# Performance work log

Measured on AMD Instinct MI355X. Metric: run time of the kernel, lower is better.

## Reference

```python
import jax, jax.numpy as jnp
import numpy as np

B, IN_CH, D, H, W = 2, 4, 8, 224, 224
DS = 4
DIM, HEADS, HEAD_DIM, LAYERS = 256, 8, 32, 4
INNER = HEADS * HEAD_DIM
MLP = 4 * DIM
WS = (4, 8, 8)
SHIFT = (2, 4, 4)
WVOL = WS[0] * WS[1] * WS[2]
Hp, Wp = H // DS, W // DS
NW = (D // WS[0]) * (Hp // WS[1]) * (Wp // WS[2])
NBIAS = (2 * WS[0] - 1) * (2 * WS[1] - 1) * (2 * WS[2] - 1)


def _rel_index():
    c = np.stack(np.meshgrid(np.arange(WS[0]), np.arange(WS[1]), np.arange(WS[2]), indexing='ij')).reshape(3, -1)
    r = (c[:, :, None] - c[:, None, :]).transpose(1, 2, 0)
    r[..., 0] += WS[0] - 1
    r[..., 1] += WS[1] - 1
    r[..., 2] += WS[2] - 1
    return r[..., 0] * (2 * WS[1] - 1) * (2 * WS[2] - 1) + r[..., 1] * (2 * WS[2] - 1) + r[..., 2]

REL_IDX = jnp.asarray(_rel_index())  # (WVOL, WVOL)


def _shift_mask():
    # standard Swin shifted-window attention mask on the post-merge grid
    img = np.zeros((D, Hp, Wp), np.int32)
    cnt = 0
    sl = lambda w, s: (slice(0, -w), slice(-w, -s), slice(-s, None))
    for sd in sl(WS[0], SHIFT[0]):
        for sh in sl(WS[1], SHIFT[1]):
            for sw in sl(WS[2], SHIFT[2]):
                img[sd, sh, sw] = cnt
                cnt += 1
    m = img.reshape(D // WS[0], WS[0], Hp // WS[1], WS[1], Wp // WS[2], WS[2])
    m = m.transpose(0, 2, 4, 1, 3, 5).reshape(NW, WVOL)
    return jnp.asarray(np.where(m[:, None, :] != m[:, :, None], -1e9, 0.0).astype(np.float32))

ATTN_MASK = _shift_mask()  # (NW, WVOL, WVOL)


def layer_norm(x, s, b):
    mu = x.mean(-1, keepdims=True)
    var = x.var(-1, keepdims=True)
    return (x - mu) / jnp.sqrt(var + 1e-5) * s + b


def window_attention(x, qkv_w, out_w, out_b, bias_tab, shifted):
    # x: (B, D, Hp, Wp, C) channel-last
    if shifted:
        x = jnp.roll(x, (-SHIFT[0], -SHIFT[1], -SHIFT[2]), axis=(1, 2, 3))
    xw = x.reshape(B, D // WS[0], WS[0], Hp // WS[1], WS[1], Wp // WS[2], WS[2], DIM)
    xw = xw.transpose(0, 1, 3, 5, 2, 4, 6, 7).reshape(B, NW, WVOL, DIM)
    qkv = xw @ qkv_w  # (B, NW, WVOL, 3*INNER)
    q, k, v = jnp.split(qkv, 3, axis=-1)
    split = lambda t: t.reshape(B, NW, WVOL, HEADS, HEAD_DIM).transpose(0, 1, 3, 2, 4)
    q = split(q) * (HEAD_DIM ** -0.5)
    k, v = split(k), split(v)
    attn = jnp.einsum('bwhid,bwhjd->bwhij', q, k)  # (B, NW, H, WVOL, WVOL)
    bias = bias_tab[REL_IDX].transpose(2, 0, 1)  # (H, WVOL, WVOL)
    attn = attn + bias
    if shifted:
        attn = attn + ATTN_MASK[None, :, None]
    attn = jax.nn.softmax(attn, axis=-1)
    o = jnp.einsum('bwhij,bwhjd->bwhid', attn, v)
    o = o.transpose(0, 1, 3, 2, 4).reshape(B, NW, WVOL, INNER)
    o = o @ out_w + out_b
    o = o.reshape(B, D // WS[0], Hp // WS[1], Wp // WS[2], WS[0], WS[1], WS[2], DIM)
    o = o.transpose(0, 1, 4, 2, 5, 3, 6, 7).reshape(B, D, Hp, Wp, DIM)
    if shifted:
        o = jnp.roll(o, SHIFT, axis=(1, 2, 3))
    return o


def setup_inputs() -> dict:
    key = jax.random.key(0)
    ks = jax.random.split(key, 12)
    s = 0.02
    return {
        'x': jax.random.normal(ks[0], (B, IN_CH, D, H, W), jnp.float32),
        'conv_w': jax.random.normal(ks[1], (DIM, IN_CH, 1, DS, DS), jnp.float32) * s,
        'conv_b': jnp.zeros((DIM,), jnp.float32),
        'ln1_s': jnp.ones((LAYERS, DIM), jnp.float32),
        'ln1_b': jnp.zeros((LAYERS, DIM), jnp.float32),
        'qkv_w': jax.random.normal(ks[2], (LAYERS, DIM, 3 * INNER), jnp.float32) * s,
        'out_w': jax.random.normal(ks[3], (LAYERS, INNER, DIM), jnp.float32) * s,
        'out_b': jnp.zeros((LAYERS, DIM), jnp.float32),
        'bias_tab': jax.random.normal(ks[4], (LAYERS, NBIAS, HEADS), jnp.float32) * s,
        'ln2_s': jnp.ones((LAYERS, DIM), jnp.float32),
        'ln2_b': jnp.zeros((LAYERS, DIM), jnp.float32),
        'fc1_w': jax.random.normal(ks[5], (LAYERS, DIM, MLP), jnp.float32) * s,
        'fc1_b': jnp.zeros((LAYERS, MLP), jnp.float32),
        'fc2_w': jax.random.normal(ks[6], (LAYERS, MLP, DIM), jnp.float32) * s,
        'fc2_b': jnp.zeros((LAYERS, DIM), jnp.float32),
    }


def reference(x, conv_w, conv_b, ln1_s, ln1_b, qkv_w, out_w, out_b, bias_tab, ln2_s, ln2_b, fc1_w, fc1_b, fc2_w, fc2_b):
    # patch merge: Conv3d kernel (1, DS, DS) stride (1, DS, DS)
    y = jax.lax.conv_general_dilated(
        x, conv_w, window_strides=(1, DS, DS), padding='VALID',
        dimension_numbers=('NCDHW', 'OIDHW', 'NCDHW'))
    y = y + conv_b[None, :, None, None, None]
    y = y.transpose(0, 2, 3, 4, 1)  # (B, D, Hp, Wp, DIM) channel-last
    for i in range(LAYERS):
        shifted = (i % 2 == 1)
        y = y + window_attention(layer_norm(y, ln1_s[i], ln1_b[i]),
                                 qkv_w[i], out_w[i], out_b[i], bias_tab[i], shifted)
        h = layer_norm(y, ln2_s[i], ln2_b[i])
        h = jax.nn.gelu(h @ fc1_w[i] + fc1_b[i]) @ fc2_w[i] + fc2_b[i]
        y = y + h
    return y.transpose(0, 4, 1, 2, 3)  # (B, DIM, D, Hp, Wp)
```

## Files before the change

kernel.cpp:

```cpp
#include <hip/hip_runtime.h>

typedef unsigned short ushort_t;
typedef unsigned int   uint_t;

#define NTOK 50176
#define NWIN 98
#define NBIAS 1575

typedef __attribute__((ext_vector_type(8))) short bf16x8;
typedef __attribute__((ext_vector_type(4))) float floatx4;

static __device__ __forceinline__ float b2f(ushort_t u) {
    return __uint_as_float(((uint_t)u) << 16);
}
static __device__ __forceinline__ ushort_t f2b(float f) {
    union { float f; uint_t u; } v; v.f = f;
    uint_t u = v.u + 0x7fffu + ((v.u >> 16) & 1u);
    return (ushort_t)(u >> 16);
}

static __device__ __forceinline__ int wtok2tok(int wt, int sh) {
    int b = wt / 25088, rem = wt - b * 25088;
    int win = rem >> 8, pos = rem & 255;
    int wd = win / 49, r1 = win - wd * 49;
    int wh = r1 / 7, ww = r1 - wh * 7;
    int d = wd * 4 + (pos >> 6), h = wh * 8 + ((pos >> 3) & 7), w = ww * 8 + (pos & 7);
    if (sh) { d = (d + 2) & 7; h += 4; if (h >= 56) h -= 56; w += 4; if (w >= 56) w -= 56; }
    return (b * 8 + d) * 3136 + h * 56 + w;
}

__global__ void transpose_w(const float* __restrict__ src, ushort_t* __restrict__ dst,
                            int K, int N) {
    long base = (long)blockIdx.y * K * N;
    int idx = blockIdx.x * 256 + threadIdx.x;
    if (idx < K * N) {
        int k = idx / N, n = idx - k * N;
        dst[base + (long)n * K + k] = f2b(src[base + idx]);
    }
}

__global__ void cast_bf16(const float* __restrict__ src, ushort_t* __restrict__ dst, int n) {
    int i = blockIdx.x * 256 + threadIdx.x;
    if (i < n) dst[i] = f2b(src[i]);
}

__global__ void expand_bias(const float* __restrict__ bias_tab, ushort_t* __restrict__ Bx) {
    int j = blockIdx.x, hd = blockIdx.y, l = blockIdx.z;
    int i = threadIdx.x;
    int rd = (i >> 6) - (j >> 6) + 3;
    int rh = ((i >> 3) & 7) - ((j >> 3) & 7) + 7;
    int rw = (i & 7) - (j & 7) + 7;
    int idx = rd * 225 + rh * 15 + rw;
    Bx[((((size_t)l * 8 + hd) << 8) + j) * 256 + i] =
        f2b(bias_tab[((size_t)l * NBIAS + idx) * 8 + hd]);
}

__global__ void im2row(const float* __restrict__ X, ushort_t* __restrict__ A) {
    int idx = blockIdx.x * 256 + threadIdx.x;
    int t = idx >> 4;
    int k = idx & 15;
    int ic = k >> 2, kh = k & 3;
    int w = t % 56, h = (t / 56) % 56, d = (t / 3136) % 8, b = t / 25088;
    long xi = (((long)(b * 4 + ic) * 8 + d) * 224 + (h * 4 + kh)) * 224 + w * 4;
    float4 u = *(const float4*)(X + xi);
    ushort_t* ap = A + (long)t * 64 + ic * 16 + kh * 4;
    ap[0] = f2b(u.x); ap[1] = f2b(u.y); ap[2] = f2b(u.z); ap[3] = f2b(u.w);
}

__global__ void ln_kernel(const float* __restrict__ Y, ushort_t* __restrict__ Xn,
                          const float* __restrict__ S, const float* __restrict__ Bb) {
    int wv = threadIdx.x >> 6, lane = threadIdx.x & 63;
    long t = (long)blockIdx.x * 4 + wv;
    const float* y = Y + t * 256;
    float v[4], s = 0.f, s2 = 0.f;
#pragma unroll
    for (int r = 0; r < 4; ++r) { v[r] = y[lane + 64 * r]; s += v[r]; s2 += v[r] * v[r]; }
#pragma unroll
    for (int off = 32; off; off >>= 1) { s += __shfl_xor(s, off, 64); s2 += __shfl_xor(s2, off, 64); }
    float mu = s * (1.f / 256.f);
    float var = s2 * (1.f / 256.f) - mu * mu;
    float rstd = rsqrtf(var + 1e-5f);
#pragma unroll
    for (int r = 0; r < 4; ++r) {
        int c = lane + 64 * r;
        Xn[t * 256 + c] = f2b((v[r] - mu) * rstd * S[c] + Bb[c]);
    }
}

__global__ __launch_bounds__(256, 2) void gemm_bt(
    const ushort_t* __restrict__ A, const ushort_t* __restrict__ BT,
    int M, int N, int K,
    const float* __restrict__ bias, int mode,
    ushort_t* __restrict__ C, float* __restrict__ Y, int sh, int asplit) {
    __shared__ ushort_t As[128 * 32];
    __shared__ ushort_t Bs[128 * 32];
    const int tid = threadIdx.x;
    const int wv = tid >> 6;
    const int lane = tid & 63;
    const int quad = lane >> 4;
    const int l15 = lane & 15;
    const long m0 = (long)blockIdx.x * 128;
    const long n0 = (long)blockIdx.y * 128;
    const int wm = (wv & 1) * 64;
    const int wn = (wv >> 1) * 64;
    const int r_loc = lane >> 2;
    const int k_loc = (lane & 3) * 8;

    floatx4 acc[4][4] = {};

    const ushort_t* Ab = A + m0 * K;
    const ushort_t* Bb = BT + n0 * K;

    for (int kt = 0; kt < K; kt += 32) {
#pragma unroll
        for (int q = 0; q < 2; ++q) {
            int slot = wv * 2 + q;
            int row = slot * 16 + r_loc;
            const ushort_t* asrc = asplit
                ? A + ((size_t)(kt >> 5) * NTOK + m0 + row) * 32 + k_loc
                : Ab + (long)row * K + kt + k_loc;
            __builtin_amdgcn_global_load_lds(
                (const __attribute__((address_space(1))) void*)asrc,
                (__attribute__((address_space(3))) void*)(As + slot * 512), 16, 0, 0);
            __builtin_amdgcn_global_load_lds(
                (const __attribute__((address_space(1))) void*)(Bb + (long)row * K + kt + k_loc),
                (__attribute__((address_space(3))) void*)(Bs + slot * 512), 16, 0, 0);
        }
        __syncthreads();
        bf16x8 af[4], bfr[4];
#pragma unroll
        for (int i = 0; i < 4; ++i) {
            af[i]  = *(const bf16x8*)(As + (wm + i * 16 + l15) * 32 + quad * 8);
            bfr[i] = *(const bf16x8*)(Bs + (wn + i * 16 + l15) * 32 + quad * 8);
        }
#pragma unroll
        for (int mi = 0; mi < 4; ++mi)
#pragma unroll
            for (int ni = 0; ni < 4; ++ni)
                acc[mi][ni] = __builtin_amdgcn_mfma_f32_16x16x32_bf16(af[mi], bfr[ni], acc[mi][ni], 0, 0, 0);
        __syncthreads();
    }

    if (mode == 2) {
#pragma unroll
        for (int mi = 0; mi < 4; ++mi)
#pragma unroll
            for (int ni = 0; ni < 4; ++ni) {
                long col = n0 + wn + ni * 16 + l15;
                float bv = bias[col];
#pragma unroll
                for (int r = 0; r < 4; ++r) {
                    long row = m0 + wm + mi * 16 + quad * 4 + r;
                    Y[row * N + col] += acc[mi][ni][r] + bv;
                }
            }
    } else if (mode == 3) {
#pragma unroll
        for (int mi = 0; mi < 4; ++mi)
#pragma unroll
            for (int ni = 0; ni < 4; ++ni) {
                long col = n0 + wn + ni * 16 + l15;
                float bv = bias[col];
#pragma unroll
                for (int r = 0; r < 4; ++r) {
                    long row = m0 + wm + mi * 16 + quad * 4 + r;
                    Y[row * N + col] = acc[mi][ni][r] + bv;
                }
            }
    } else if (mode == 4) {
#pragma unroll
        for (int mi = 0; mi < 4; ++mi)
#pragma unroll
            for (int ni = 0; ni < 4; ++ni) {
                int c = (int)(n0 + wn + ni * 16 + l15);
                int seg = c >> 5, ch = c & 31;
                ushort_t* base = C + ((size_t)seg * NTOK) * 32 + ch;
#pragma unroll
                for (int r = 0; r < 4; ++r) {
                    size_t row = (size_t)(m0 + wm + mi * 16 + quad * 4 + r);
                    base[row * 32] = f2b(acc[mi][ni][r]);
                }
            }
    } else if (mode == 5) {
#pragma unroll
        for (int mi = 0; mi < 4; ++mi) {
            int tk[4];
#pragma unroll
            for (int r = 0; r < 4; ++r)
                tk[r] = wtok2tok((int)(m0 + wm + mi * 16 + quad * 4 + r), sh);
#pragma unroll
            for (int ni = 0; ni < 4; ++ni) {
                long col = n0 + wn + ni * 16 + l15;
                float bv = bias[col];
#pragma unroll
                for (int r = 0; r < 4; ++r)
                    Y[(size_t)tk[r] * N + col] += acc[mi][ni][r] + bv;
            }
        }
    } else {
#pragma unroll
        for (int mi = 0; mi < 4; ++mi)
#pragma unroll
            for (int ni = 0; ni < 4; ++ni) {
                long col = n0 + wn + ni * 16 + l15;
                float bv = bias ? bias[col] : 0.f;
#pragma unroll
                for (int r = 0; r < 4; ++r) {
                    long row = m0 + wm + mi * 16 + quad * 4 + r;
                    float v = acc[mi][ni][r] + bv;
                    if (mode == 1) {
                        float x3 = v * v * v;
                        v = 0.5f * v * (1.f + tanhf(0.7978845608028654f * (v + 0.044715f * x3)));
                    }
                    C[row * N + col] = f2b(v);
                }
            }
    }
}

#define VTS 268
#define OLS 34
__global__ __launch_bounds__(256, 4) void attn_mfma(
    const ushort_t* __restrict__ QKV, ushort_t* __restrict__ O,
    const ushort_t* __restrict__ Bx, int shifted) {
    __shared__ ushort_t Ks[256 * 32];
    __shared__ ushort_t Vt[32 * VTS];
    __shared__ ushort_t Ol[4 * 16 * OLS];
    __shared__ int tok_s[256];
    __shared__ int reg_s[256];

    const int tid = threadIdx.x;
    const int wv = tid >> 6;
    const int lane = tid & 63;
    const int quad = lane >> 4;
    const int l15 = lane & 15;
    const int hd = blockIdx.x, win = blockIdx.y, b = blockIdx.z;
    const int wd = win / 49, r1w = win - wd * 49;
    const int wh = r1w / 7, ww = r1w - wh * 7;
    const size_t wbase = ((size_t)b * 98 + win) * 256;
    const ushort_t* Qg = QKV + (size_t)hd * NTOK * 32;
    const ushort_t* Kg = QKV + (size_t)(8 + hd) * NTOK * 32;
    const ushort_t* Vg = QKV + (size_t)(16 + hd) * NTOK * 32;

    {
        int pos = tid;
        int d = wd * 4 + (pos >> 6), h = wh * 8 + ((pos >> 3) & 7), w = ww * 8 + (pos & 7);
        int rd = d < 4 ? 0 : (d < 6 ? 1 : 2);
        int rh = h < 48 ? 0 : (h < 52 ? 1 : 2);
        int rw = w < 48 ? 0 : (w < 52 ? 1 : 2);
        reg_s[pos] = rd * 9 + rh * 3 + rw;
        int d0 = d, h0 = h, w0 = w;
        if (shifted) { d0 = (d + 2) & 7; h0 = h + 4; if (h0 >= 56) h0 -= 56; w0 = w + 4; if (w0 >= 56) w0 -= 56; }
        tok_s[pos] = (b * 8 + d0) * 3136 + h0 * 56 + w0;
    }
    __syncthreads();
    {
#pragma unroll
        for (int q = 0; q < 4; ++q) {
            int t = wv * 64 + q * 16 + (lane >> 2);
            const ushort_t* src = Kg + (size_t)tok_s[t] * 32 + (lane & 3) * 8;
            __builtin_amdgcn_global_load_lds(
                (const __attribute__((address_space(1))) void*)src,
                (__attribute__((address_space(3))) void*)(Ks + wv * 2048 + q * 512), 16, 0, 0);
        }
#pragma unroll
        for (int p = 0; p < 4; ++p) {
            int u = tid + p * 256;
            int tok = u >> 2, chb = (u & 3) * 8;
            uint4 vv = *(const uint4*)(Vg + (size_t)tok_s[tok] * 32 + chb);
            uint_t uu[4] = {vv.x, vv.y, vv.z, vv.w};
#pragma unroll
            for (int e = 0; e < 4; ++e) {
                Vt[(chb + 2 * e) * VTS + tok]     = (ushort_t)(uu[e] & 0xffffu);
                Vt[(chb + 2 * e + 1) * VTS + tok] = (ushort_t)(uu[e] >> 16);
            }
        }
    }
    __syncthreads();

    const int hm = shifted && (wd == 1 || wh == 6 || ww == 6);
    const float scale = 0.17677669529663687f;
    const ushort_t* bb = Bx + ((size_t)hd << 16) + l15;
    ushort_t* ow = Ol + wv * 16 * OLS;
    ushort_t* Og = O + ((size_t)hd * NTOK + wbase) * 32;

    for (int rg = 0; rg < 4; ++rg) {
        const int q0 = (wv * 4 + rg) * 16;
        bf16x8 aq;
        {
            union { uint4 u; bf16x8 v; } cv;
            cv.u = *(const uint4*)(Qg + (size_t)tok_s[q0 + l15] * 32 + quad * 8);
            aq = cv.v;
        }
        floatx4 Sc[16];
#pragma unroll
        for (int nt = 0; nt < 16; ++nt) {
            bf16x8 bk = *(const bf16x8*)(Ks + (nt * 16 + l15) * 32 + quad * 8);
            floatx4 z = {};
            Sc[nt] = __builtin_amdgcn_mfma_f32_16x16x32_bf16(bk, aq, z, 0, 0, 0);
        }
        float mx = -3e38f;
        const ushort_t* bq = bb + q0;
        if (!hm) {
#pragma unroll
            for (int nt = 0; nt < 16; ++nt)
#pragma unroll
                for (int r = 0; r < 4; ++r) {
                    float s = fmaf(Sc[nt][r], scale, b2f(bq[(nt * 16 + quad * 4 + r) << 8]));
                    Sc[nt][r] = s; mx = fmaxf(mx, s);
                }
        } else {
            int myreg = reg_s[q0 + l15];
#pragma unroll
            for (int nt = 0; nt < 16; ++nt)
#pragma unroll
                for (int r = 0; r < 4; ++r) {
                    int key = nt * 16 + quad * 4 + r;
                    float s = fmaf(Sc[nt][r], scale, b2f(bq[key << 8]));
                    s = (reg_s[key] == myreg) ? s : -1e9f;
                    Sc[nt][r] = s; mx = fmaxf(mx, s);
                }
        }
        mx = fmaxf(mx, __shfl_xor(mx, 16, 64));
        mx = fmaxf(mx, __shfl_xor(mx, 32, 64));
        float lsum = 0.f;
#pragma unroll
        for (int nt = 0; nt < 16; ++nt)
#pragma unroll
            for (int r = 0; r < 4; ++r) {
                float p = __expf(Sc[nt][r] - mx);
                lsum += p; Sc[nt][r] = p;
            }
        lsum += __shfl_xor(lsum, 16, 64);
        lsum += __shfl_xor(lsum, 32, 64);
        float inv = 1.f / lsum;
        floatx4 oc[2] = {{0.f,0.f,0.f,0.f},{0.f,0.f,0.f,0.f}};
        const ushort_t* vr = Vt + quad * 4;
#pragma unroll
        for (int kt = 0; kt < 8; ++kt) {
            union { uint_t u[4]; bf16x8 v; } bp;
            bp.u[0] = __builtin_amdgcn_perm(__float_as_uint(Sc[2*kt][1]),   __float_as_uint(Sc[2*kt][0]),   0x07060302u);
            bp.u[1] = __builtin_amdgcn_perm(__float_as_uint(Sc[2*kt][3]),   __float_as_uint(Sc[2*kt][2]),   0x07060302u);
            bp.u[2] = __builtin_amdgcn_perm(__float_as_uint(Sc[2*kt+1][1]), __float_as_uint(Sc[2*kt+1][0]), 0x07060302u);
            bp.u[3] = __builtin_amdgcn_perm(__float_as_uint(Sc[2*kt+1][3]), __float_as_uint(Sc[2*kt+1][2]), 0x07060302u);
#pragma unroll
            for (int ct = 0; ct < 2; ++ct) {
                const ushort_t* vrow = vr + (ct * 16 + l15) * VTS;
                union { unsigned long long l[2]; bf16x8 v; } av;
                av.l[0] = *(const unsigned long long*)(vrow + 2 * kt * 16);
                av.l[1] = *(const unsigned long long*)(vrow + 2 * kt * 16 + 16);
                oc[ct] = __builtin_amdgcn_mfma_f32_16x16x32_bf16(av.v, bp.v, oc[ct], 0, 0, 0);
            }
        }
#pragma unroll
        for (int ct = 0; ct < 2; ++ct) {
            uint2 st;
            st.x = (uint_t)f2b(oc[ct][0] * inv) | ((uint_t)f2b(oc[ct][1] * inv) << 16);
            st.y = (uint_t)f2b(oc[ct][2] * inv) | ((uint_t)f2b(oc[ct][3] * inv) << 16);
            *(uint2*)(ow + l15 * OLS + ct * 16 + quad * 4) = st;
        }
        __builtin_amdgcn_s_waitcnt(0xC07F);
        __builtin_amdgcn_wave_barrier();
        {
            int qr = lane >> 2, chk = (lane & 3) * 8;
            uint4 val = *(const uint4*)(ow + qr * OLS + chk);
            *(uint4*)(Og + (size_t)(q0 + qr) * 32 + chk) = val;
        }
        __builtin_amdgcn_wave_barrier();
    }
}

__global__ void out_permute(const float* __restrict__ Y, float* __restrict__ Out) {
    __shared__ float tile[64][65];
    const int t0 = blockIdx.x * 64;
    const int c0 = blockIdx.y * 64;
    const int tid = threadIdx.x;
    const int a = tid >> 6;
    const int bx = tid & 63;
#pragma unroll
    for (int s8 = 0; s8 < 16; ++s8) {
        int tt = a + s8 * 4;
        tile[tt][bx] = Y[(long)(t0 + tt) * 256 + c0 + bx];
    }
    __syncthreads();
#pragma unroll
    for (int s8 = 0; s8 < 16; ++s8) {
        int cc = a + s8 * 4;
        int tok = t0 + bx;
        int bb = tok / 25088;
        int rem = tok - bb * 25088;
        Out[((long)(bb * 256 + c0 + cc)) * 25088 + rem] = tile[bx][cc];
    }
}

extern "C" void kernel_launch(void* const* d_in, const int* in_sizes, int n_in,
                              void* d_out, int out_size, void* d_ws, size_t ws_size,
                              hipStream_t stream) {
    (void)in_sizes; (void)n_in; (void)out_size; (void)ws_size;
    const float* x        = (const float*)d_in[0];
    const float* conv_w   = (const float*)d_in[1];
    const float* conv_b   = (const float*)d_in[2];
    const float* ln1_s    = (const float*)d_in[3];
    const float* ln1_b    = (const float*)d_in[4];
    const float* qkv_w    = (const float*)d_in[5];
    const float* out_w    = (const float*)d_in[6];
    const float* out_b    = (const float*)d_in[7];
    const float* bias_tab = (const float*)d_in[8];
    const float* ln2_s    = (const float*)d_in[9];
    const float* ln2_b    = (const float*)d_in[10];
    const float* fc1_w    = (const float*)d_in[11];
    const float* fc1_b    = (const float*)d_in[12];
    const float* fc2_w    = (const float*)d_in[13];
    const float* fc2_b    = (const float*)d_in[14];
    float* out = (float*)d_out;

    char* ws = (char*)d_ws;
    float*    y    = (float*)ws;    ws += (size_t)NTOK * 256 * 4;
    ushort_t* big  = (ushort_t*)ws; ws += (size_t)NTOK * 1024 * 2;
    ushort_t* xob  = (ushort_t*)ws; ws += (size_t)NTOK * 256 * 2;
    ushort_t* bt_qkv = (ushort_t*)ws; ws += (size_t)4 * 768 * 256 * 2;
    ushort_t* bt_out = (ushort_t*)ws; ws += (size_t)4 * 256 * 256 * 2;
    ushort_t* bt_fc1 = (ushort_t*)ws; ws += (size_t)4 * 1024 * 256 * 2;
    ushort_t* bt_fc2 = (ushort_t*)ws; ws += (size_t)4 * 256 * 1024 * 2;
    ushort_t* cw_bf  = (ushort_t*)ws; ws += (size_t)256 * 64 * 2;
    ushort_t* Bx     = (ushort_t*)ws; ws += (size_t)4 * 8 * 256 * 256 * 2;

    transpose_w<<<dim3((256 * 768 + 255) / 256, 4), 256, 0, stream>>>(qkv_w, bt_qkv, 256, 768);
    transpose_w<<<dim3((256 * 256 + 255) / 256, 4), 256, 0, stream>>>(out_w, bt_out, 256, 256);
    transpose_w<<<dim3((256 * 1024 + 255) / 256, 4), 256, 0, stream>>>(fc1_w, bt_fc1, 256, 1024);
    transpose_w<<<dim3((1024 * 256 + 255) / 256, 4), 256, 0, stream>>>(fc2_w, bt_fc2, 1024, 256);
    expand_bias<<<dim3(256, 8, 4), 256, 0, stream>>>(bias_tab, Bx);

    cast_bf16<<<(256 * 64 + 255) / 256, 256, 0, stream>>>(conv_w, cw_bf, 256 * 64);
    im2row<<<NTOK * 16 / 256, 256, 0, stream>>>(x, big);
    gemm_bt<<<dim3(NTOK / 128, 2), 256, 0, stream>>>(
        big, cw_bf, NTOK, 256, 64, conv_b, 3, nullptr, y, 0, 0);

    for (int i = 0; i < 4; ++i) {
        int sh = i & 1;
        ln_kernel<<<NTOK / 4, 256, 0, stream>>>(y, xob, ln1_s + i * 256, ln1_b + i * 256);
        gemm_bt<<<dim3(NTOK / 128, 6), 256, 0, stream>>>(
            xob, bt_qkv + (size_t)i * 768 * 256, NTOK, 768, 256, nullptr, 4, big, nullptr, 0, 0);
        attn_mfma<<<dim3(8, NWIN, 2), 256, 0, stream>>>(
            big, xob, Bx + (size_t)i * 8 * 65536, sh);
        gemm_bt<<<dim3(NTOK / 128, 2), 256, 0, stream>>>(
            xob, bt_out + (size_t)i * 256 * 256, NTOK, 256, 256, out_b + i * 256, 5, nullptr, y, sh, 1);
        ln_kernel<<<NTOK / 4, 256, 0, stream>>>(y, xob, ln2_s + i * 256, ln2_b + i * 256);
        gemm_bt<<<dim3(NTOK / 128, 8), 256, 0, stream>>>(
            xob, bt_fc1 + (size_t)i * 1024 * 256, NTOK, 1024, 256, fc1_b + i * 1024, 1, big, nullptr, 0, 0);
        gemm_bt<<<dim3(NTOK / 128, 2), 256, 0, stream>>>(
            big, bt_fc2 + (size_t)i * 256 * 1024, NTOK, 256, 1024, fc2_b + i * 256, 2, nullptr, y, 0, 0);
    }

    out_permute<<<dim3(NTOK / 64, 4), 256, 0, stream>>>(y, out);
}
```

Before: 1.477 ms.

## Scatter attention output to token order and compute rel-pos bias from table in LDS

The attention kernel now writes its output directly in token-major layout at the un-shifted token positions, so the output-projection GEMM becomes a plain contiguous GEMM with residual add instead of a split-A load plus window-to-token scatter epilogue. The expanded 256x256 bf16 bias per head and layer is dropped. Each attention block instead loads the 1575-entry bias table for its head into LDS and indexes it arithmetically, removing the expand_bias kernel and a large bias read stream. GELU's tanh form is rewritten as an equivalent x*sigmoid(2z) using __expf. The cost is scattered 8-byte global stores from the attention kernel and small per-block table loads.

```diff
diff --git a/kernel.cpp b/kernel.cpp
--- a/kernel.cpp
+++ b/kernel.cpp
@@ -17,16 +17,6 @@
     union { float f; uint_t u; } v; v.f = f;
     uint_t u = v.u + 0x7fffu + ((v.u >> 16) & 1u);
     return (ushort_t)(u >> 16);
-}
-
-static __device__ __forceinline__ int wtok2tok(int wt, int sh) {
-    int b = wt / 25088, rem = wt - b * 25088;
-    int win = rem >> 8, pos = rem & 255;
-    int wd = win / 49, r1 = win - wd * 49;
-    int wh = r1 / 7, ww = r1 - wh * 7;
-    int d = wd * 4 + (pos >> 6), h = wh * 8 + ((pos >> 3) & 7), w = ww * 8 + (pos & 7);
-    if (sh) { d = (d + 2) & 7; h += 4; if (h >= 56) h -= 56; w += 4; if (w >= 56) w -= 56; }
-    return (b * 8 + d) * 3136 + h * 56 + w;
 }
 
 __global__ void transpose_w(const float* __restrict__ src, ushort_t* __restrict__ dst,
@@ -42,17 +32,6 @@
 __global__ void cast_bf16(const float* __restrict__ src, ushort_t* __restrict__ dst, int n) {
     int i = blockIdx.x * 256 + threadIdx.x;
     if (i < n) dst[i] = f2b(src[i]);
-}
-
-__global__ void expand_bias(const float* __restrict__ bias_tab, ushort_t* __restrict__ Bx) {
-    int j = blockIdx.x, hd = blockIdx.y, l = blockIdx.z;
-    int i = threadIdx.x;
-    int rd = (i >> 6) - (j >> 6) + 3;
-    int rh = ((i >> 3) & 7) - ((j >> 3) & 7) + 7;
-    int rw = (i & 7) - (j & 7) + 7;
-    int idx = rd * 225 + rh * 15 + rw;
-    Bx[((((size_t)l * 8 + hd) << 8) + j) * 256 + i] =
-        f2b(bias_tab[((size_t)l * NBIAS + idx) * 8 + hd]);
 }
 
 __global__ void im2row(const float* __restrict__ X, ushort_t* __restrict__ A) {
@@ -91,7 +70,7 @@
     const ushort_t* __restrict__ A, const ushort_t* __restrict__ BT,
     int M, int N, int K,
     const float* __restrict__ bias, int mode,
-    ushort_t* __restrict__ C, float* __restrict__ Y, int sh, int asplit) {
+    ushort_t* __restrict__ C, float* __restrict__ Y) {
     __shared__ ushort_t As[128 * 32];
     __shared__ ushort_t Bs[128 * 32];
     const int tid = threadIdx.x;
@@ -116,11 +95,8 @@
         for (int q = 0; q < 2; ++q) {
             int slot = wv * 2 + q;
             int row = slot * 16 + r_loc;
-            const ushort_t* asrc = asplit
-                ? A + ((size_t)(kt >> 5) * NTOK + m0 + row) * 32 + k_loc
-                : Ab + (long)row * K + kt + k_loc;
             __builtin_amdgcn_global_load_lds(
-                (const __attribute__((address_space(1))) void*)asrc,
+                (const __attribute__((address_space(1))) void*)(Ab + (long)row * K + kt + k_loc),
                 (__attribute__((address_space(3))) void*)(As + slot * 512), 16, 0, 0);
             __builtin_amdgcn_global_load_lds(
                 (const __attribute__((address_space(1))) void*)(Bb + (long)row * K + kt + k_loc),
@@ -181,22 +157,6 @@
                     base[row * 32] = f2b(acc[mi][ni][r]);
                 }
             }
-    } else if (mode == 5) {
-#pragma unroll
-        for (int mi = 0; mi < 4; ++mi) {
-            int tk[4];
-#pragma unroll
-            for (int r = 0; r < 4; ++r)
-                tk[r] = wtok2tok((int)(m0 + wm + mi * 16 + quad * 4 + r), sh);
-#pragma unroll
-            for (int ni = 0; ni < 4; ++ni) {
-                long col = n0 + wn + ni * 16 + l15;
-                float bv = bias[col];
-#pragma unroll
-                for (int r = 0; r < 4; ++r)
-                    Y[(size_t)tk[r] * N + col] += acc[mi][ni][r] + bv;
-            }
-        }
     } else {
 #pragma unroll
         for (int mi = 0; mi < 4; ++mi)
@@ -209,8 +169,8 @@
                     long row = m0 + wm + mi * 16 + quad * 4 + r;
                     float v = acc[mi][ni][r] + bv;
                     if (mode == 1) {
-                        float x3 = v * v * v;
-                        v = 0.5f * v * (1.f + tanhf(0.7978845608028654f * (v + 0.044715f * x3)));
+                        float z2 = 1.5957691216057308f * (v + 0.044715f * v * v * v);
+                        v = v / (1.f + __expf(-z2));
                     }
                     C[row * N + col] = f2b(v);
                 }
@@ -219,13 +179,12 @@
 }
 
 #define VTS 268
-#define OLS 34
 __global__ __launch_bounds__(256, 4) void attn_mfma(
     const ushort_t* __restrict__ QKV, ushort_t* __restrict__ O,
-    const ushort_t* __restrict__ Bx, int shifted) {
+    const float* __restrict__ bias_tab, int shifted) {
     __shared__ ushort_t Ks[256 * 32];
     __shared__ ushort_t Vt[32 * VTS];
-    __shared__ ushort_t Ol[4 * 16 * OLS];
+    __shared__ ushort_t bias_s[1576];
     __shared__ int tok_s[256];
     __shared__ int reg_s[256];
 
@@ -237,7 +196,6 @@
     const int hd = blockIdx.x, win = blockIdx.y, b = blockIdx.z;
     const int wd = win / 49, r1w = win - wd * 49;
     const int wh = r1w / 7, ww = r1w - wh * 7;
-    const size_t wbase = ((size_t)b * 98 + win) * 256;
     const ushort_t* Qg = QKV + (size_t)hd * NTOK * 32;
     const ushort_t* Kg = QKV + (size_t)(8 + hd) * NTOK * 32;
     const ushort_t* Vg = QKV + (size_t)(16 + hd) * NTOK * 32;
@@ -253,6 +211,7 @@
         if (shifted) { d0 = (d + 2) & 7; h0 = h + 4; if (h0 >= 56) h0 -= 56; w0 = w + 4; if (w0 >= 56) w0 -= 56; }
         tok_s[pos] = (b * 8 + d0) * 3136 + h0 * 56 + w0;
     }
+    for (int r = tid; r < NBIAS; r += 256) bias_s[r] = f2b(bias_tab[r * 8 + hd]);
     __syncthreads();
     {
 #pragma unroll
@@ -280,16 +239,16 @@
 
     const int hm = shifted && (wd == 1 || wh == 6 || ww == 6);
     const float scale = 0.17677669529663687f;
-    const ushort_t* bb = Bx + ((size_t)hd << 16) + l15;
-    ushort_t* ow = Ol + wv * 16 * OLS;
-    ushort_t* Og = O + ((size_t)hd * NTOK + wbase) * 32;
 
     for (int rg = 0; rg < 4; ++rg) {
         const int q0 = (wv * 4 + rg) * 16;
+        const int qpos = q0 + l15;
+        const int qb2 = (qpos >> 6) * 225 + ((qpos >> 3) & 7) * 15 + (qpos & 7) + 787
+                        - (quad >> 1) * 15 - (quad & 1) * 4;
         bf16x8 aq;
         {
             union { uint4 u; bf16x8 v; } cv;
-            cv.u = *(const uint4*)(Qg + (size_t)tok_s[q0 + l15] * 32 + quad * 8);
+            cv.u = *(const uint4*)(Qg + (size_t)tok_s[qpos] * 32 + quad * 8);
             aq = cv.v;
         }
         floatx4 Sc[16];
@@ -300,26 +259,29 @@
             Sc[nt] = __builtin_amdgcn_mfma_f32_16x16x32_bf16(bk, aq, z, 0, 0, 0);
         }
         float mx = -3e38f;
-        const ushort_t* bq = bb + q0;
         if (!hm) {
 #pragma unroll
-            for (int nt = 0; nt < 16; ++nt)
-#pragma unroll
-                for (int r = 0; r < 4; ++r) {
-                    float s = fmaf(Sc[nt][r], scale, b2f(bq[(nt * 16 + quad * 4 + r) << 8]));
+            for (int nt = 0; nt < 16; ++nt) {
+                const int knt = (nt >> 2) * 225 + (nt & 3) * 30;
+#pragma unroll
+                for (int r = 0; r < 4; ++r) {
+                    float s = fmaf(Sc[nt][r], scale, b2f(bias_s[qb2 - knt - r]));
                     Sc[nt][r] = s; mx = fmaxf(mx, s);
                 }
+            }
         } else {
-            int myreg = reg_s[q0 + l15];
-#pragma unroll
-            for (int nt = 0; nt < 16; ++nt)
+            int myreg = reg_s[qpos];
+#pragma unroll
+            for (int nt = 0; nt < 16; ++nt) {
+                const int knt = (nt >> 2) * 225 + (nt & 3) * 30;
 #pragma unroll
                 for (int r = 0; r < 4; ++r) {
                     int key = nt * 16 + quad * 4 + r;
-                    float s = fmaf(Sc[nt][r], scale, b2f(bq[key << 8]));
+                    float s = fmaf(Sc[nt][r], scale, b2f(bias_s[qb2 - knt - r]));
                     s = (reg_s[key] == myreg) ? s : -1e9f;
                     Sc[nt][r] = s; mx = fmaxf(mx, s);
                 }
+            }
         }
         mx = fmaxf(mx, __shfl_xor(mx, 16, 64));
         mx = fmaxf(mx, __shfl_xor(mx, 32, 64));
@@ -352,21 +314,16 @@
                 oc[ct] = __builtin_amdgcn_mfma_f32_16x16x32_bf16(av.v, bp.v, oc[ct], 0, 0, 0);
             }
         }
-#pragma unroll
-        for (int ct = 0; ct < 2; ++ct) {
-            uint2 st;
-            st.x = (uint_t)f2b(oc[ct][0] * inv) | ((uint_t)f2b(oc[ct][1] * inv) << 16);
-            st.y = (uint_t)f2b(oc[ct][2] * inv) | ((uint_t)f2b(oc[ct][3] * inv) << 16);
-            *(uint2*)(ow + l15 * OLS + ct * 16 + quad * 4) = st;
-        }
-        __builtin_amdgcn_s_waitcnt(0xC07F);
-        __builtin_amdgcn_wave_barrier();
         {
-            int qr = lane >> 2, chk = (lane & 3) * 8;
-            uint4 val = *(const uint4*)(ow + qr * OLS + chk);
-            *(uint4*)(Og + (size_t)(q0 + qr) * 32 + chk) = val;
-        }
-        __builtin_amdgcn_wave_barrier();
+            size_t obase = (size_t)tok_s[qpos] * 256 + hd * 32 + quad * 4;
+#pragma unroll
+            for (int ct = 0; ct < 2; ++ct) {
+                uint2 st;
+                st.x = (uint_t)f2b(oc[ct][0] * inv) | ((uint_t)f2b(oc[ct][1] * inv) << 16);
+                st.y = (uint_t)f2b(oc[ct][2] * inv) | ((uint_t)f2b(oc[ct][3] * inv) << 16);
+                *(uint2*)(O + obase + ct * 16) = st;
+            }
+        }
     }
 }
 
@@ -423,33 +380,31 @@
     ushort_t* bt_fc1 = (ushort_t*)ws; ws += (size_t)4 * 1024 * 256 * 2;
     ushort_t* bt_fc2 = (ushort_t*)ws; ws += (size_t)4 * 256 * 1024 * 2;
     ushort_t* cw_bf  = (ushort_t*)ws; ws += (size_t)256 * 64 * 2;
-    ushort_t* Bx     = (ushort_t*)ws; ws += (size_t)4 * 8 * 256 * 256 * 2;
 
     transpose_w<<<dim3((256 * 768 + 255) / 256, 4), 256, 0, stream>>>(qkv_w, bt_qkv, 256, 768);
     transpose_w<<<dim3((256 * 256 + 255) / 256, 4), 256, 0, stream>>>(out_w, bt_out, 256, 256);
     transpose_w<<<dim3((256 * 1024 + 255) / 256, 4), 256, 0, stream>>>(fc1_w, bt_fc1, 256, 1024);
     transpose_w<<<dim3((1024 * 256 + 255) / 256, 4), 256, 0, stream>>>(fc2_w, bt_fc2, 1024, 256);
-    expand_bias<<<dim3(256, 8, 4), 256, 0, stream>>>(bias_tab, Bx);
 
     cast_bf16<<<(256 * 64 + 255) / 256, 256, 0, stream>>>(conv_w, cw_bf, 256 * 64);
     im2row<<<NTOK * 16 / 256, 256, 0, stream>>>(x, big);
     gemm_bt<<<dim3(NTOK / 128, 2), 256, 0, stream>>>(
-        big, cw_bf, NTOK, 256, 64, conv_b, 3, nullptr, y, 0, 0);
+        big, cw_bf, NTOK, 256, 64, conv_b, 3, nullptr, y);
 
     for (int i = 0; i < 4; ++i) {
         int sh = i & 1;
         ln_kernel<<<NTOK / 4, 256, 0, stream>>>(y, xob, ln1_s + i * 256, ln1_b + i * 256);
         gemm_bt<<<dim3(NTOK / 128, 6), 256, 0, stream>>>(
-            xob, bt_qkv + (size_t)i * 768 * 256, NTOK, 768, 256, nullptr, 4, big, nullptr, 0, 0);
+            xob, bt_qkv + (size_t)i * 768 * 256, NTOK, 768, 256, nullptr, 4, big, nullptr);
         attn_mfma<<<dim3(8, NWIN, 2), 256, 0, stream>>>(
-            big, xob, Bx + (size_t)i * 8 * 65536, sh);
+            big, xob, bias_tab + (size_t)i * NBIAS * 8, sh);
         gemm_bt<<<dim3(NTOK / 128, 2), 256, 0, stream>>>(
-            xob, bt_out + (size_t)i * 256 * 256, NTOK, 256, 256, out_b + i * 256, 5, nullptr, y, sh, 1);
+            xob, bt_out + (size_t)i * 256 * 256, NTOK, 256, 256, out_b + i * 256, 2, nullptr, y);
         ln_kernel<<<NTOK / 4, 256, 0, stream>>>(y, xob, ln2_s + i * 256, ln2_b + i * 256);
         gemm_bt<<<dim3(NTOK / 128, 8), 256, 0, stream>>>(
-            xob, bt_fc1 + (size_t)i * 1024 * 256, NTOK, 1024, 256, fc1_b + i * 1024, 1, big, nullptr, 0, 0);
+            xob, bt_fc1 + (size_t)i * 1024 * 256, NTOK, 1024, 256, fc1_b + i * 1024, 1, big, nullptr);
         gemm_bt<<<dim3(NTOK / 128, 2), 256, 0, stream>>>(
-            big, bt_fc2 + (size_t)i * 256 * 1024, NTOK, 256, 1024, fc2_b + i * 256, 2, nullptr, y, 0, 0);
+            big, bt_fc2 + (size_t)i * 256 * 1024, NTOK, 256, 1024, fc2_b + i * 256, 2, nullptr, y);
     }
 
     out_permute<<<dim3(NTOK / 64, 4), 256, 0, stream>>>(y, out);
```

Result: slower. 2.385 ms (+61.5%).
